# Performance work log

Measured on AMD Instinct MI355X. Metric: run time of the kernel, lower is better.

## Reference

```python
import jax, jax.numpy as jnp
import numpy as np

B, T, I = 256, 384, 32      # batch, seq_len, input_size
M, D, O = 128, 64, 128      # ring positions, embedding_dim, num_outputs
K = 2                       # attention_radius -> 2K+1 = 5 neighbors
TEMP = 8.0                  # attention_temperature
EPS = 1e-5                  # torch LayerNorm default eps


def setup_inputs() -> dict:
    key = jax.random.key(0)
    ks = jax.random.split(key, 12)
    def lin(kw, kb, fan_in, shape_w, shape_b):
        lim = 1.0 / np.sqrt(fan_in)
        W = jax.random.uniform(kw, shape_w, jnp.float32, -lim, lim)
        b = jax.random.uniform(kb, shape_b, jnp.float32, -lim, lim)
        return W, b
    Wp, bp = lin(ks[0], ks[1], I, (I, D), (D,))
    Wg, bg = lin(ks[2], ks[3], D, (D, 1), (1,))
    Wo, bo = lin(ks[4], ks[5], D, (D, O), (O,))
    return {
        "x": jax.random.normal(ks[6], (B, T, I), jnp.float32),
        "ptr_init": jax.random.uniform(ks[7], (B,), jnp.float32) * M,
        "Wp": Wp, "bp": bp,
        "gamma": jnp.ones((D,), jnp.float32),
        "beta": jnp.zeros((D,), jnp.float32),
        "jump_dest": jax.random.uniform(ks[8], (M,), jnp.float32) * M,
        "Wg": Wg, "bg": bg,
        "ctx_strength": jnp.asarray(0.2, jnp.float32),
        "Wo": Wo, "bo": bo,
    }


def reference(x, ptr_init, Wp, bp, gamma, beta, jump_dest, Wg, bg, ctx_strength, Wo, bo):
    offsets = jnp.arange(-K, K + 1)               # [2K+1]
    bidx = jnp.arange(B)[:, None]                 # [B,1] batch index for gather/scatter
    half = M / 2.0
    ctx_scale = jax.nn.sigmoid(ctx_strength)

    def step(carry, x_t):
        ring, hidden, ptr = carry                 # [B,M,D], [B,D], [B]
        emb = jnp.tanh(x_t @ Wp + bp)             # input projection + activation
        # Gaussian attention over circular neighborhood of floor(ptr)
        base = jnp.clip(jnp.floor(ptr).astype(jnp.int32), 0, M - 1)
        idx = (base[:, None] + offsets[None, :]) % M            # [B,2K+1]
        delta = jnp.mod(idx.astype(ptr.dtype) - ptr[:, None] + half, M) - half
        w = jax.nn.softmax(-(delta ** 2) / TEMP, axis=1)        # [B,2K+1]
        neigh = ring[bidx, idx]                                  # gather [B,2K+1,D]
        ctx = jnp.sum(w[:, :, None] * neigh, axis=1)             # [B,D]
        state = jnp.tanh(emb + ctx_scale * ctx + hidden)
        # LayerNorm (biased variance, affine)
        mu = jnp.mean(state, axis=-1, keepdims=True)
        var = jnp.var(state, axis=-1, keepdims=True)
        hidden_new = (state - mu) * jax.lax.rsqrt(var + EPS) * gamma + beta
        # scatter-add weighted state back into the ring
        ring = ring.at[bidx, idx].add(w[:, :, None] * state[:, None, :])
        # pointer update: hard STE gate between learned jump and +1 walk
        cur = jnp.clip(ptr.astype(jnp.int32), 0, M - 1)
        jump_target = jump_dest[cur]
        jl = (state @ Wg + bg)[:, 0]
        probs = jax.nn.sigmoid(jl)
        gate = (probs > 0.5).astype(state.dtype) - jax.lax.stop_gradient(probs) + probs
        walk = (ptr + 1.0) % M
        ptr_new = jnp.where(gate > 0.5, jump_target, walk)
        return (ring, hidden_new, ptr_new), None

    ring0 = jnp.zeros((B, M, D), x.dtype)
    h0 = jnp.zeros((B, D), x.dtype)
    (ring, hidden, ptr), _ = jax.lax.scan(step, (ring0, h0, ptr_init), jnp.swapaxes(x, 0, 1))
    logits = hidden @ Wo + bo                     # [B, O]
    return logits
```

## Files before the change

kernel.cpp:

```cpp
#include <hip/hip_runtime.h>
#include <hip/hip_bf16.h>


#define BB 256
#define TT 384
#define II 32
#define MM 128
#define DD 64
#define OO 128
#define K2 0.1803368801f
#define L2E2 2.885390082f
#define IL2E2 0.3465735903f
#define PR 133
#define CHK 8
#define NCHK (TT / CHK)
#define NSLOT 6

__device__ __forceinline__ float bfbits(unsigned int lo16) {
    return __uint_as_float(lo16 << 16);
}
__device__ __forceinline__ float ldf(const void* p, long long i, bool isbf) {
    if (isbf) return bfbits((unsigned int)((const unsigned short*)p)[i]);
    return ((const float*)p)[i];
}

template <int CTRL>
__device__ __forceinline__ float dpp_add(float x) {
    int s = __builtin_amdgcn_update_dpp(0, __float_as_int(x), CTRL, 0xf, 0xf, true);
    return x + __int_as_float(s);
}
__device__ __forceinline__ void reduce3(float& a, float& b, float& c) {
    a = dpp_add<0x111>(a); b = dpp_add<0x111>(b); c = dpp_add<0x111>(c);
    a = dpp_add<0x112>(a); b = dpp_add<0x112>(b); c = dpp_add<0x112>(c);
    a = dpp_add<0x114>(a); b = dpp_add<0x114>(b); c = dpp_add<0x114>(c);
    a = dpp_add<0x118>(a); b = dpp_add<0x118>(b); c = dpp_add<0x118>(c);
    a = dpp_add<0x142>(a); b = dpp_add<0x142>(b); c = dpp_add<0x142>(c);
    a = dpp_add<0x143>(a); b = dpp_add<0x143>(b); c = dpp_add<0x143>(c);
    a = __int_as_float(__builtin_amdgcn_readlane(__float_as_int(a), 63));
    b = __int_as_float(__builtin_amdgcn_readlane(__float_as_int(b), 63));
    c = __int_as_float(__builtin_amdgcn_readlane(__float_as_int(c), 63));
}

__device__ __forceinline__ float fast_tanh(float x) {
    float e = __builtin_amdgcn_exp2f(x * L2E2);
    return fmaf(-2.0f, __builtin_amdgcn_rcpf(e + 1.0f), 1.0f);
}

__global__ __launch_bounds__(256, 1)
void ring_fused(const void* __restrict__ x,
                const void* __restrict__ ptr_init,
                const void* __restrict__ Wp,
                const void* __restrict__ bp,
                const void* __restrict__ gamma,
                const void* __restrict__ beta,
                const void* __restrict__ jump_dest,
                const void* __restrict__ Wg,
                const void* __restrict__ bg,
                const void* __restrict__ cs,
                const void* __restrict__ Wo,
                const void* __restrict__ bo,
                void* __restrict__ out)
{
    __shared__ __align__(16) float ring[PR * DD];
    __shared__ __align__(16) float ebuf[NSLOT * CHK * DD];
    __shared__ __align__(16) float tab[MM * 8];
    __shared__ float hsh[DD];
    __shared__ int chunk_ready[NCHK];
    __shared__ int cons_done;

    const int tid = threadIdx.x;
    const int wid = tid >> 6;
    const int lane = tid & 63;
    const int b = blockIdx.x;
    const bool isbf = (((const unsigned int*)gamma)[0] == 0x3f803f80u);

    if (tid < NCHK) chunk_ready[tid] = 0;
    if (tid == 0) cons_done = 0;
    __syncthreads();

    if (wid != 0) {
        float wp[II];
        #pragma unroll
        for (int k = 0; k < II; k++) wp[k] = ldf(Wp, k * DD + lane, isbf);
        const float bpv = ldf(bp, lane, isbf);
        volatile int* vcd = &cons_done;

        for (int c = wid - 1; c < NCHK; c += 3) {
            while (*vcd < c - (NSLOT - 1)) __builtin_amdgcn_s_sleep(8);
            float* eslot = ebuf + (c % NSLOT) * (CHK * DD);
            #pragma unroll
            for (int k = 0; k < CHK; k++) {
                const size_t t = (size_t)c * CHK + k;
                float acc = bpv;
                if (isbf) {
                    const uint4* xr = (const uint4*)
                        ((const unsigned short*)x + ((size_t)b * TT + t) * II);
                    #pragma unroll
                    for (int q = 0; q < 4; q++) {
                        uint4 u = xr[q];
                        unsigned int uu[4] = {u.x, u.y, u.z, u.w};
                        #pragma unroll
                        for (int e = 0; e < 4; e++) {
                            acc = fmaf(bfbits(uu[e] & 0xffffu), wp[q * 8 + e * 2], acc);
                            acc = fmaf(bfbits(uu[e] >> 16),     wp[q * 8 + e * 2 + 1], acc);
                        }
                    }
                } else {
                    const float4* xr = (const float4*)
                        ((const float*)x + ((size_t)b * TT + t) * II);
                    #pragma unroll
                    for (int q = 0; q < II / 4; q++) {
                        float4 v = xr[q];
                        acc = fmaf(v.x, wp[q * 4 + 0], acc);
                        acc = fmaf(v.y, wp[q * 4 + 1], acc);
                        acc = fmaf(v.z, wp[q * 4 + 2], acc);
                        acc = fmaf(v.w, wp[q * 4 + 3], acc);
                    }
                }
                eslot[k * DD + lane] = fast_tanh(acc);
            }
            __threadfence_block();
            if (lane == 0) *(volatile int*)&chunk_ready[c] = 1;
        }
        return;
    }

    {
        float4 z4 = make_float4(0.f, 0.f, 0.f, 0.f);
        #pragma unroll
        for (int i = 0; i < 33; i++)
            ((float4*)ring)[lane + i * 64] = z4;
        ring[8448 + lane] = 0.0f;
    }

    const float gam = ldf(gamma, lane, isbf);
    const float bet = ldf(beta, lane, isbf);
    const float wgv = ldf(Wg, lane, isbf);
    const float bg64 = ldf(bg, 0, isbf) * (1.0f / 64.0f);
    const float csv = 1.0f / (1.0f + expf(-ldf(cs, 0, isbf)));
    const float csv2 = csv * L2E2;
    const float gam2 = gam * L2E2;
    const float bet2 = bet * L2E2;

    #pragma unroll
    for (int h = 0; h < 2; h++) {
        const int m = lane + h * 64;
        const float jd = ldf(jump_dest, m, isbf);
        int bj = (int)jd; bj = min(bj, MM - 1);
        const float fj = jd - (float)bj;
        float e[5], se = 0.0f;
        #pragma unroll
        for (int j = 0; j < 5; j++) {
            const float dd = (float)(j - 2) - fj;
            e[j] = __builtin_amdgcn_exp2f(dd * dd * -K2);
            se += e[j];
        }
        const float inv = __builtin_amdgcn_rcpf(se);
        #pragma unroll
        for (int j = 0; j < 5; j++) tab[m * 8 + j] = e[j] * inv;
        tab[m * 8 + 5] = __int_as_float(bj);
    }

    const float p0 = ldf(ptr_init, b, isbf);
    int sbase = __builtin_amdgcn_readfirstlane(min(max((int)floorf(p0), 0), MM - 1));
    const float frac = p0 - (float)sbase;
    float w0, w1, w2, w3, w4;
    {
        float e[5], se = 0.0f;
        #pragma unroll
        for (int j = 0; j < 5; j++) {
            const float dd = (float)(j - 2) - frac;
            e[j] = __builtin_amdgcn_exp2f(dd * dd * -K2);
            se += e[j];
        }
        const float inv = __builtin_amdgcn_rcpf(se);
        w0 = e[0] * inv; w1 = e[1] * inv; w2 = e[2] * inv;
        w3 = e[3] * inv; w4 = e[4] * inv;
    }

    float nb0 = 0.f, nb1 = 0.f, nb2 = 0.f, nb3 = 0.f, nb4 = 0.f;
    float dg = -bet2, rstd = 1.0f;
    volatile int* vcr = chunk_ready;

    for (int c = 0; c < NCHK; c++) {
        while (!vcr[c]) __builtin_amdgcn_s_sleep(1);
        const float* eslot = ebuf + (c % NSLOT) * (CHK * DD);

        float evb2[CHK];
        #pragma unroll
        for (int j = 0; j < CHK; j++)
            evb2[j] = fmaf(eslot[j * DD + lane], L2E2, bet2);

        #pragma unroll
        for (int k = 0; k < CHK; k++) {
            const float* ce = tab + (sbase << 3);
            const float c0 = ce[0], c1 = ce[1], c2 = ce[2],
                        c3 = ce[3], c4 = ce[4];
            const int bjc = __float_as_int(ce[5]);
            float* rb = ring + sbase * DD + lane;
            const float W5p = rb[5 * DD];

            const float ctx = fmaf(w0, nb0, fmaf(w1, nb1, 0.0f)) +
                              fmaf(w2, nb2, fmaf(w3, nb3, w4 * nb4));
            const float A  = fmaf(dg, rstd, evb2[k]);
            const float ex = __builtin_amdgcn_exp2f(fmaf(csv2, ctx, A));
            const float sn = fmaf(-2.0f, __builtin_amdgcn_rcpf(ex + 1.0f), 1.0f);

            float r0 = sn, r1 = sn * sn, r2 = fmaf(sn, wgv, bg64);
            reduce3(r0, r1, r2);

            const float nv0 = fmaf(w0, sn, nb0), nv1 = fmaf(w1, sn, nb1),
                        nv2 = fmaf(w2, sn, nb2), nv3 = fmaf(w3, sn, nb3),
                        nv4 = fmaf(w4, sn, nb4);
            rb[0 * DD] = nv0; rb[1 * DD] = nv1; rb[2 * DD] = nv2;
            rb[3 * DD] = nv3; rb[4 * DD] = nv4;
            if (sbase <= 4 || sbase >= MM - 4) {
                const float nvv[5] = {nv0, nv1, nv2, nv3, nv4};
                #pragma unroll
                for (int j = 0; j < 5; j++) {
                    const int p = sbase + j;
                    if (p < 5)        ring[(p + MM) * DD + lane] = nvv[j];
                    else if (p >= MM) ring[(p - MM) * DD + lane] = nvv[j];
                }
            }

            const float mu = r0 * (1.0f / 64.0f);
            const float q  = fmaf(r1, 1.0f / 64.0f, 1e-5f);
            const float va = fmaf(-mu, mu, q);
            rstd = __builtin_amdgcn_rsqf(va);
            dg = (sn - mu) * gam2;

            if (__float_as_int(r2) > 0) {
                w0 = c0; w1 = c1; w2 = c2; w3 = c3; w4 = c4;
                sbase = __builtin_amdgcn_readfirstlane(bjc);
                const float* rj = ring + sbase * DD + lane;
                nb0 = rj[0 * DD]; nb1 = rj[1 * DD]; nb2 = rj[2 * DD];
                nb3 = rj[3 * DD]; nb4 = rj[4 * DD];
            } else {
                nb0 = nv1; nb1 = nv2; nb2 = nv3; nb3 = nv4; nb4 = W5p;
                sbase = (sbase + 1) & (MM - 1);
            }
        }
        if (lane == 0) *(volatile int*)&cons_done = c + 1;
    }

    const float hid_raw = fmaf(dg * rstd, IL2E2, bet);
    hsh[lane] = hid_raw;
    float a0 = ldf(bo, lane, isbf);
    float a1 = ldf(bo, lane + 64, isbf);
    #pragma unroll 8
    for (int d = 0; d < DD; d++) {
        const float h = hsh[d];
        a0 = fmaf(h, ldf(Wo, d * OO + lane, isbf), a0);
        a1 = fmaf(h, ldf(Wo, d * OO + lane + 64, isbf), a1);
    }
    if (isbf) {
        __hip_bfloat16* o = (__hip_bfloat16*)out;
        o[(size_t)b * OO + lane] = __float2bfloat16(a0);
        o[(size_t)b * OO + lane + 64] = __float2bfloat16(a1);
    } else {
        float* o = (float*)out;
        o[(size_t)b * OO + lane] = a0;
        o[(size_t)b * OO + lane + 64] = a1;
    }
}

extern "C" void kernel_launch(void* const* d_in, const int* in_sizes, int n_in,
                              void* d_out, int out_size, void* d_ws, size_t ws_size,
                              hipStream_t stream) {
    ring_fused<<<BB, 256, 0, stream>>>(
        d_in[0], d_in[1], d_in[2], d_in[3], d_in[4], d_in[5],
        d_in[6], d_in[7], d_in[8], d_in[9], d_in[10], d_in[11], d_out);
}
```

Baseline: 190.3 us.

## Process two batch rows per block with interleaved recurrences

Each workgroup now handles two batch elements, with separate rings and embedding buffers. The consumer wave interleaves the two serial recurrences and merges their wave reductions into one six-value DPP reduction. The aim is to hide the latency of the dependent per-step chain with instruction-level parallelism. The cost is halving the grid to 128 blocks, which leaves half the CUs idle, and doubling LDS use and producer work per block.

```diff
diff --git a/kernel.cpp b/kernel.cpp
--- a/kernel.cpp
+++ b/kernel.cpp
@@ -29,16 +29,19 @@
     int s = __builtin_amdgcn_update_dpp(0, __float_as_int(x), CTRL, 0xf, 0xf, true);
     return x + __int_as_float(s);
 }
-__device__ __forceinline__ void reduce3(float& a, float& b, float& c) {
-    a = dpp_add<0x111>(a); b = dpp_add<0x111>(b); c = dpp_add<0x111>(c);
-    a = dpp_add<0x112>(a); b = dpp_add<0x112>(b); c = dpp_add<0x112>(c);
-    a = dpp_add<0x114>(a); b = dpp_add<0x114>(b); c = dpp_add<0x114>(c);
-    a = dpp_add<0x118>(a); b = dpp_add<0x118>(b); c = dpp_add<0x118>(c);
-    a = dpp_add<0x142>(a); b = dpp_add<0x142>(b); c = dpp_add<0x142>(c);
-    a = dpp_add<0x143>(a); b = dpp_add<0x143>(b); c = dpp_add<0x143>(c);
+#define R6STAGE(CTRL) \
+    a = dpp_add<CTRL>(a); b = dpp_add<CTRL>(b); c = dpp_add<CTRL>(c); \
+    d = dpp_add<CTRL>(d); e = dpp_add<CTRL>(e); f = dpp_add<CTRL>(f);
+__device__ __forceinline__ void reduce6(float& a, float& b, float& c,
+                                        float& d, float& e, float& f) {
+    R6STAGE(0x111) R6STAGE(0x112) R6STAGE(0x114)
+    R6STAGE(0x118) R6STAGE(0x142) R6STAGE(0x143)
     a = __int_as_float(__builtin_amdgcn_readlane(__float_as_int(a), 63));
     b = __int_as_float(__builtin_amdgcn_readlane(__float_as_int(b), 63));
     c = __int_as_float(__builtin_amdgcn_readlane(__float_as_int(c), 63));
+    d = __int_as_float(__builtin_amdgcn_readlane(__float_as_int(d), 63));
+    e = __int_as_float(__builtin_amdgcn_readlane(__float_as_int(e), 63));
+    f = __int_as_float(__builtin_amdgcn_readlane(__float_as_int(f), 63));
 }
 
 __device__ __forceinline__ float fast_tanh(float x) {
@@ -61,17 +64,20 @@
                 const void* __restrict__ bo,
                 void* __restrict__ out)
 {
-    __shared__ __align__(16) float ring[PR * DD];
-    __shared__ __align__(16) float ebuf[NSLOT * CHK * DD];
+    __shared__ __align__(16) float ringA[PR * DD];
+    __shared__ __align__(16) float ringB[PR * DD];
+    __shared__ __align__(16) float ebufA[NSLOT * CHK * DD];
+    __shared__ __align__(16) float ebufB[NSLOT * CHK * DD];
     __shared__ __align__(16) float tab[MM * 8];
-    __shared__ float hsh[DD];
+    __shared__ float hsh[2 * DD];
     __shared__ int chunk_ready[NCHK];
     __shared__ int cons_done;
 
     const int tid = threadIdx.x;
     const int wid = tid >> 6;
     const int lane = tid & 63;
-    const int b = blockIdx.x;
+    const int bA = blockIdx.x * 2;
+    const int bB = bA + 1;
     const bool isbf = (((const unsigned int*)gamma)[0] == 0x3f803f80u);
 
     if (tid < NCHK) chunk_ready[tid] = 0;
@@ -87,37 +93,41 @@
 
         for (int c = wid - 1; c < NCHK; c += 3) {
             while (*vcd < c - (NSLOT - 1)) __builtin_amdgcn_s_sleep(8);
-            float* eslot = ebuf + (c % NSLOT) * (CHK * DD);
             #pragma unroll
-            for (int k = 0; k < CHK; k++) {
-                const size_t t = (size_t)c * CHK + k;
-                float acc = bpv;
-                if (isbf) {
-                    const uint4* xr = (const uint4*)
-                        ((const unsigned short*)x + ((size_t)b * TT + t) * II);
-                    #pragma unroll
-                    for (int q = 0; q < 4; q++) {
-                        uint4 u = xr[q];
-                        unsigned int uu[4] = {u.x, u.y, u.z, u.w};
+            for (int bb = 0; bb < 2; bb++) {
+                const int b = bb ? bB : bA;
+                float* eslot = (bb ? ebufB : ebufA) + (c % NSLOT) * (CHK * DD);
+                #pragma unroll
+                for (int k = 0; k < CHK; k++) {
+                    const size_t t = (size_t)c * CHK + k;
+                    float acc = bpv;
+                    if (isbf) {
+                        const uint4* xr = (const uint4*)
+                            ((const unsigned short*)x + ((size_t)b * TT + t) * II);
                         #pragma unroll
-                        for (int e = 0; e < 4; e++) {
-                            acc = fmaf(bfbits(uu[e] & 0xffffu), wp[q * 8 + e * 2], acc);
-                            acc = fmaf(bfbits(uu[e] >> 16),     wp[q * 8 + e * 2 + 1], acc);
+                        for (int q = 0; q < 4; q++) {
+                            uint4 u = xr[q];
+                            unsigned int uu[4] = {u.x, u.y, u.z, u.w};
+                            #pragma unroll
+                            for (int e = 0; e < 4; e++) {
+                                acc = fmaf(bfbits(uu[e] & 0xffffu), wp[q * 8 + e * 2], acc);
+                                acc = fmaf(bfbits(uu[e] >> 16),     wp[q * 8 + e * 2 + 1], acc);
+                            }
+                        }
+                    } else {
+                        const float4* xr = (const float4*)
+                            ((const float*)x + ((size_t)b * TT + t) * II);
+                        #pragma unroll
+                        for (int q = 0; q < II / 4; q++) {
+                            float4 v = xr[q];
+                            acc = fmaf(v.x, wp[q * 4 + 0], acc);
+                            acc = fmaf(v.y, wp[q * 4 + 1], acc);
+                            acc = fmaf(v.z, wp[q * 4 + 2], acc);
+                            acc = fmaf(v.w, wp[q * 4 + 3], acc);
                         }
                     }
-                } else {
-                    const float4* xr = (const float4*)
-                        ((const float*)x + ((size_t)b * TT + t) * II);
-                    #pragma unroll
-                    for (int q = 0; q < II / 4; q++) {
-                        float4 v = xr[q];
-                        acc = fmaf(v.x, wp[q * 4 + 0], acc);
-                        acc = fmaf(v.y, wp[q * 4 + 1], acc);
-                        acc = fmaf(v.z, wp[q * 4 + 2], acc);
-                        acc = fmaf(v.w, wp[q * 4 + 3], acc);
-                    }
+                    eslot[k * DD + lane] = fast_tanh(acc);
                 }
-                eslot[k * DD + lane] = fast_tanh(acc);
             }
             __threadfence_block();
             if (lane == 0) *(volatile int*)&chunk_ready[c] = 1;
@@ -128,9 +138,12 @@
     {
         float4 z4 = make_float4(0.f, 0.f, 0.f, 0.f);
         #pragma unroll
-        for (int i = 0; i < 33; i++)
-            ((float4*)ring)[lane + i * 64] = z4;
-        ring[8448 + lane] = 0.0f;
+        for (int i = 0; i < 33; i++) {
+            ((float4*)ringA)[lane + i * 64] = z4;
+            ((float4*)ringB)[lane + i * 64] = z4;
+        }
+        ringA[8448 + lane] = 0.0f;
+        ringB[8448 + lane] = 0.0f;
     }
 
     const float gam = ldf(gamma, lane, isbf);
@@ -161,11 +174,12 @@
         tab[m * 8 + 5] = __int_as_float(bj);
     }
 
-    const float p0 = ldf(ptr_init, b, isbf);
-    int sbase = __builtin_amdgcn_readfirstlane(min(max((int)floorf(p0), 0), MM - 1));
-    const float frac = p0 - (float)sbase;
-    float w0, w1, w2, w3, w4;
+    int sbaseA, sbaseB;
+    float wA0, wA1, wA2, wA3, wA4, wB0, wB1, wB2, wB3, wB4;
     {
+        const float p0 = ldf(ptr_init, bA, isbf);
+        sbaseA = __builtin_amdgcn_readfirstlane(min(max((int)floorf(p0), 0), MM - 1));
+        const float frac = p0 - (float)sbaseA;
         float e[5], se = 0.0f;
         #pragma unroll
         for (int j = 0; j < 5; j++) {
@@ -174,101 +188,177 @@
             se += e[j];
         }
         const float inv = __builtin_amdgcn_rcpf(se);
-        w0 = e[0] * inv; w1 = e[1] * inv; w2 = e[2] * inv;
-        w3 = e[3] * inv; w4 = e[4] * inv;
-    }
-
-    float nb0 = 0.f, nb1 = 0.f, nb2 = 0.f, nb3 = 0.f, nb4 = 0.f;
-    float dg = -bet2, rstd = 1.0f;
+        wA0 = e[0] * inv; wA1 = e[1] * inv; wA2 = e[2] * inv;
+        wA3 = e[3] * inv; wA4 = e[4] * inv;
+    }
+    {
+        const float p0 = ldf(ptr_init, bB, isbf);
+        sbaseB = __builtin_amdgcn_readfirstlane(min(max((int)floorf(p0), 0), MM - 1));
+        const float frac = p0 - (float)sbaseB;
+        float e[5], se = 0.0f;
+        #pragma unroll
+        for (int j = 0; j < 5; j++) {
+            const float dd = (float)(j - 2) - frac;
+            e[j] = __builtin_amdgcn_exp2f(dd * dd * -K2);
+            se += e[j];
+        }
+        const float inv = __builtin_amdgcn_rcpf(se);
+        wB0 = e[0] * inv; wB1 = e[1] * inv; wB2 = e[2] * inv;
+        wB3 = e[3] * inv; wB4 = e[4] * inv;
+    }
+
+    float nbA0 = 0.f, nbA1 = 0.f, nbA2 = 0.f, nbA3 = 0.f, nbA4 = 0.f;
+    float nbB0 = 0.f, nbB1 = 0.f, nbB2 = 0.f, nbB3 = 0.f, nbB4 = 0.f;
+    float dgA = -bet2, rstdA = 1.0f;
+    float dgB = -bet2, rstdB = 1.0f;
     volatile int* vcr = chunk_ready;
 
     for (int c = 0; c < NCHK; c++) {
         while (!vcr[c]) __builtin_amdgcn_s_sleep(1);
-        const float* eslot = ebuf + (c % NSLOT) * (CHK * DD);
-
-        float evb2[CHK];
-        #pragma unroll
-        for (int j = 0; j < CHK; j++)
-            evb2[j] = fmaf(eslot[j * DD + lane], L2E2, bet2);
+        const float* eslotA = ebufA + (c % NSLOT) * (CHK * DD);
+        const float* eslotB = ebufB + (c % NSLOT) * (CHK * DD);
+
+        float evb2A[CHK], evb2B[CHK];
+        #pragma unroll
+        for (int j = 0; j < CHK; j++) {
+            evb2A[j] = fmaf(eslotA[j * DD + lane], L2E2, bet2);
+            evb2B[j] = fmaf(eslotB[j * DD + lane], L2E2, bet2);
+        }
 
         #pragma unroll
         for (int k = 0; k < CHK; k++) {
-            const float* ce = tab + (sbase << 3);
-            const float c0 = ce[0], c1 = ce[1], c2 = ce[2],
-                        c3 = ce[3], c4 = ce[4];
-            const int bjc = __float_as_int(ce[5]);
-            float* rb = ring + sbase * DD + lane;
-            const float W5p = rb[5 * DD];
-
-            const float ctx = fmaf(w0, nb0, fmaf(w1, nb1, 0.0f)) +
-                              fmaf(w2, nb2, fmaf(w3, nb3, w4 * nb4));
-            const float A  = fmaf(dg, rstd, evb2[k]);
-            const float ex = __builtin_amdgcn_exp2f(fmaf(csv2, ctx, A));
-            const float sn = fmaf(-2.0f, __builtin_amdgcn_rcpf(ex + 1.0f), 1.0f);
-
-            float r0 = sn, r1 = sn * sn, r2 = fmaf(sn, wgv, bg64);
-            reduce3(r0, r1, r2);
-
-            const float nv0 = fmaf(w0, sn, nb0), nv1 = fmaf(w1, sn, nb1),
-                        nv2 = fmaf(w2, sn, nb2), nv3 = fmaf(w3, sn, nb3),
-                        nv4 = fmaf(w4, sn, nb4);
-            rb[0 * DD] = nv0; rb[1 * DD] = nv1; rb[2 * DD] = nv2;
-            rb[3 * DD] = nv3; rb[4 * DD] = nv4;
-            if (sbase <= 4 || sbase >= MM - 4) {
-                const float nvv[5] = {nv0, nv1, nv2, nv3, nv4};
+            const float* ceA = tab + (sbaseA << 3);
+            const float cA0 = ceA[0], cA1 = ceA[1], cA2 = ceA[2],
+                        cA3 = ceA[3], cA4 = ceA[4];
+            const int bjcA = __float_as_int(ceA[5]);
+            float* rbA = ringA + sbaseA * DD + lane;
+            const float W5pA = rbA[5 * DD];
+            const float ctxA = fmaf(wA0, nbA0, fmaf(wA1, nbA1, 0.0f)) +
+                               fmaf(wA2, nbA2, fmaf(wA3, nbA3, wA4 * nbA4));
+            const float AA = fmaf(dgA, rstdA, evb2A[k]);
+            const float exA = __builtin_amdgcn_exp2f(fmaf(csv2, ctxA, AA));
+            const float snA = fmaf(-2.0f, __builtin_amdgcn_rcpf(exA + 1.0f), 1.0f);
+
+            const float* ceB = tab + (sbaseB << 3);
+            const float cB0 = ceB[0], cB1 = ceB[1], cB2 = ceB[2],
+                        cB3 = ceB[3], cB4 = ceB[4];
+            const int bjcB = __float_as_int(ceB[5]);
+            float* rbB = ringB + sbaseB * DD + lane;
+            const float W5pB = rbB[5 * DD];
+            const float ctxB = fmaf(wB0, nbB0, fmaf(wB1, nbB1, 0.0f)) +
+                               fmaf(wB2, nbB2, fmaf(wB3, nbB3, wB4 * nbB4));
+            const float AB = fmaf(dgB, rstdB, evb2B[k]);
+            const float exB = __builtin_amdgcn_exp2f(fmaf(csv2, ctxB, AB));
+            const float snB = fmaf(-2.0f, __builtin_amdgcn_rcpf(exB + 1.0f), 1.0f);
+
+            const float nvA0 = fmaf(wA0, snA, nbA0), nvA1 = fmaf(wA1, snA, nbA1),
+                        nvA2 = fmaf(wA2, snA, nbA2), nvA3 = fmaf(wA3, snA, nbA3),
+                        nvA4 = fmaf(wA4, snA, nbA4);
+            rbA[0 * DD] = nvA0; rbA[1 * DD] = nvA1; rbA[2 * DD] = nvA2;
+            rbA[3 * DD] = nvA3; rbA[4 * DD] = nvA4;
+            if (sbaseA <= 4 || sbaseA >= MM - 4) {
+                const float nvv[5] = {nvA0, nvA1, nvA2, nvA3, nvA4};
                 #pragma unroll
                 for (int j = 0; j < 5; j++) {
-                    const int p = sbase + j;
-                    if (p < 5)        ring[(p + MM) * DD + lane] = nvv[j];
-                    else if (p >= MM) ring[(p - MM) * DD + lane] = nvv[j];
+                    const int p = sbaseA + j;
+                    if (p < 5)        ringA[(p + MM) * DD + lane] = nvv[j];
+                    else if (p >= MM) ringA[(p - MM) * DD + lane] = nvv[j];
                 }
             }
 
-            const float mu = r0 * (1.0f / 64.0f);
-            const float q  = fmaf(r1, 1.0f / 64.0f, 1e-5f);
-            const float va = fmaf(-mu, mu, q);
-            rstd = __builtin_amdgcn_rsqf(va);
-            dg = (sn - mu) * gam2;
-
-            if (__float_as_int(r2) > 0) {
-                w0 = c0; w1 = c1; w2 = c2; w3 = c3; w4 = c4;
-                sbase = __builtin_amdgcn_readfirstlane(bjc);
-                const float* rj = ring + sbase * DD + lane;
-                nb0 = rj[0 * DD]; nb1 = rj[1 * DD]; nb2 = rj[2 * DD];
-                nb3 = rj[3 * DD]; nb4 = rj[4 * DD];
+            const float nvB0 = fmaf(wB0, snB, nbB0), nvB1 = fmaf(wB1, snB, nbB1),
+                        nvB2 = fmaf(wB2, snB, nbB2), nvB3 = fmaf(wB3, snB, nbB3),
+                        nvB4 = fmaf(wB4, snB, nbB4);
+            rbB[0 * DD] = nvB0; rbB[1 * DD] = nvB1; rbB[2 * DD] = nvB2;
+            rbB[3 * DD] = nvB3; rbB[4 * DD] = nvB4;
+            if (sbaseB <= 4 || sbaseB >= MM - 4) {
+                const float nvv[5] = {nvB0, nvB1, nvB2, nvB3, nvB4};
+                #pragma unroll
+                for (int j = 0; j < 5; j++) {
+                    const int p = sbaseB + j;
+                    if (p < 5)        ringB[(p + MM) * DD + lane] = nvv[j];
+                    else if (p >= MM) ringB[(p - MM) * DD + lane] = nvv[j];
+                }
+            }
+
+            float r0A = snA, r1A = snA * snA, r2A = fmaf(snA, wgv, bg64);
+            float r0B = snB, r1B = snB * snB, r2B = fmaf(snB, wgv, bg64);
+            reduce6(r0A, r1A, r2A, r0B, r1B, r2B);
+
+            const float muA = r0A * (1.0f / 64.0f);
+            const float qA  = fmaf(r1A, 1.0f / 64.0f, 1e-5f);
+            const float vaA = fmaf(-muA, muA, qA);
+            rstdA = __builtin_amdgcn_rsqf(vaA);
+            dgA = (snA - muA) * gam2;
+
+            const float muB = r0B * (1.0f / 64.0f);
+            const float qB  = fmaf(r1B, 1.0f / 64.0f, 1e-5f);
+            const float vaB = fmaf(-muB, muB, qB);
+            rstdB = __builtin_amdgcn_rsqf(vaB);
+            dgB = (snB - muB) * gam2;
+
+            if (__float_as_int(r2A) > 0) {
+                wA0 = cA0; wA1 = cA1; wA2 = cA2; wA3 = cA3; wA4 = cA4;
+                sbaseA = __builtin_amdgcn_readfirstlane(bjcA);
+                const float* rj = ringA + sbaseA * DD + lane;
+                nbA0 = rj[0 * DD]; nbA1 = rj[1 * DD]; nbA2 = rj[2 * DD];
+                nbA3 = rj[3 * DD]; nbA4 = rj[4 * DD];
             } else {
-                nb0 = nv1; nb1 = nv2; nb2 = nv3; nb3 = nv4; nb4 = W5p;
-                sbase = (sbase + 1) & (MM - 1);
+                nbA0 = nvA1; nbA1 = nvA2; nbA2 = nvA3; nbA3 = nvA4; nbA4 = W5pA;
+                sbaseA = (sbaseA + 1) & (MM - 1);
+            }
+
+            if (__float_as_int(r2B) > 0) {
+                wB0 = cB0; wB1 = cB1; wB2 = cB2; wB3 = cB3; wB4 = cB4;
+                sbaseB = __builtin_amdgcn_readfirstlane(bjcB);
+                const float* rj = ringB + sbaseB * DD + lane;
+                nbB0 = rj[0 * DD]; nbB1 = rj[1 * DD]; nbB2 = rj[2 * DD];
+                nbB3 = rj[3 * DD]; nbB4 = rj[4 * DD];
+            } else {
+                nbB0 = nvB1; nbB1 = nvB2; nbB2 = nvB3; nbB3 = nvB4; nbB4 = W5pB;
+                sbaseB = (sbaseB + 1) & (MM - 1);
             }
         }
         if (lane == 0) *(volatile int*)&cons_done = c + 1;
     }
 
-    const float hid_raw = fmaf(dg * rstd, IL2E2, bet);
-    hsh[lane] = hid_raw;
-    float a0 = ldf(bo, lane, isbf);
-    float a1 = ldf(bo, lane + 64, isbf);
+    const float hidA = fmaf(dgA * rstdA, IL2E2, bet);
+    const float hidB = fmaf(dgB * rstdB, IL2E2, bet);
+    hsh[lane] = hidA;
+    hsh[DD + lane] = hidB;
+    const float bo0 = ldf(bo, lane, isbf);
+    const float bo1 = ldf(bo, lane + 64, isbf);
+    float a0A = bo0, a1A = bo1, a0B = bo0, a1B = bo1;
     #pragma unroll 8
     for (int d = 0; d < DD; d++) {
-        const float h = hsh[d];
-        a0 = fmaf(h, ldf(Wo, d * OO + lane, isbf), a0);
-        a1 = fmaf(h, ldf(Wo, d * OO + lane + 64, isbf), a1);
+        const float hA = hsh[d];
+        const float hB = hsh[DD + d];
+        const float wo0 = ldf(Wo, d * OO + lane, isbf);
+        const float wo1 = ldf(Wo, d * OO + lane + 64, isbf);
+        a0A = fmaf(hA, wo0, a0A);
+        a1A = fmaf(hA, wo1, a1A);
+        a0B = fmaf(hB, wo0, a0B);
+        a1B = fmaf(hB, wo1, a1B);
     }
     if (isbf) {
         __hip_bfloat16* o = (__hip_bfloat16*)out;
-        o[(size_t)b * OO + lane] = __float2bfloat16(a0);
-        o[(size_t)b * OO + lane + 64] = __float2bfloat16(a1);
+        o[(size_t)bA * OO + lane] = __float2bfloat16(a0A);
+        o[(size_t)bA * OO + lane + 64] = __float2bfloat16(a1A);
+        o[(size_t)bB * OO + lane] = __float2bfloat16(a0B);
+        o[(size_t)bB * OO + lane + 64] = __float2bfloat16(a1B);
     } else {
         float* o = (float*)out;
-        o[(size_t)b * OO + lane] = a0;
-        o[(size_t)b * OO + lane + 64] = a1;
+        o[(size_t)bA * OO + lane] = a0A;
+        o[(size_t)bA * OO + lane + 64] = a1A;
+        o[(size_t)bB * OO + lane] = a0B;
+        o[(size_t)bB * OO + lane + 64] = a1B;
     }
 }
 
 extern "C" void kernel_launch(void* const* d_in, const int* in_sizes, int n_in,
                               void* d_out, int out_size, void* d_ws, size_t ws_size,
                               hipStream_t stream) {
-    ring_fused<<<BB, 256, 0, stream>>>(
+    ring_fused<<<BB / 2, 256, 0, stream>>>(
         d_in[0], d_in[1], d_in[2], d_in[3], d_in[4], d_in[5],
         d_in[6], d_in[7], d_in[8], d_in[9], d_in[10], d_in[11], d_out);
 }
```

Result: slower. 278.8 us (+46.5%).
